# Performance work log

Measured on AMD Instinct MI355X. Metric: run time of the kernel, lower is better.

## Reference

```python
import jax, jax.numpy as jnp
import numpy as np
import math

D_HEAD = 64  # scaling uses sqrt(d_head), NOT sqrt of full projection dim (faithful to source)

def setup_inputs() -> dict:
    key = jax.random.key(0)
    ks = jax.random.split(key, 9)
    B, S, D = 4, 2048, 1024
    s = 0.02
    return {
        "x": jax.random.normal(ks[0], (B, S, D), dtype=jnp.float32),
        "Wq": jax.random.normal(ks[1], (D, D), dtype=jnp.float32) * s,
        "bq": jax.random.normal(ks[2], (D,), dtype=jnp.float32) * s,
        "Wk": jax.random.normal(ks[3], (D, D), dtype=jnp.float32) * s,
        "bk": jax.random.normal(ks[4], (D,), dtype=jnp.float32) * s,
        "Wv": jax.random.normal(ks[5], (D, D), dtype=jnp.float32) * s,
        "bv": jax.random.normal(ks[6], (D,), dtype=jnp.float32) * s,
        "Wo": jax.random.normal(ks[7], (D, D), dtype=jnp.float32) * s,
        "bo": jax.random.normal(ks[8], (D,), dtype=jnp.float32) * s,
    }

def reference(x, Wq, bq, Wk, bk, Wv, bv, Wo, bo):
    # Q/K/V projections: [B,S,D] @ [D,D] + b
    Q = jnp.einsum('bsd,de->bse', x, Wq) + bq
    K = jnp.einsum('bsd,de->bse', x, Wk) + bk
    V = jnp.einsum('bsd,de->bse', x, Wv) + bv
    # NOTE: source does bmm over the FULL projected dim (no head split),
    # scaled by sqrt(d_head) only.
    scores = jnp.einsum('bqd,bkd->bqk', Q, K) / math.sqrt(D_HEAD)  # [B,S,S]
    S_len = scores.shape[-1]
    causal = jnp.tril(jnp.ones((S_len, S_len), dtype=bool))
    scores = jnp.where(causal, scores, -jnp.inf)
    weights = jax.nn.softmax(scores, axis=-1)
    attn_out = jnp.einsum('bqk,bkd->bqd', weights, V)
    return jnp.einsum('bsd,de->bse', attn_out, Wo) + bo
```

## Files before the change

kernel.cpp:

```cpp
#include <hip/hip_runtime.h>
#include <stdint.h>

typedef _Float16 f16;
typedef __attribute__((ext_vector_type(8))) _Float16 f16x8;
typedef __attribute__((ext_vector_type(4))) _Float16 f16x4;
typedef __attribute__((ext_vector_type(4))) float f32x4;

#define BK 32

typedef __attribute__((address_space(3))) uint32_t lds_u32;
typedef const __attribute__((address_space(1))) uint32_t glb_u32;

__device__ __forceinline__ void gload_lds16(const void* g, void* l) {
    __builtin_amdgcn_global_load_lds((glb_u32*)g, (lds_u32*)l, 16, 0, 0);
}

template<int OUT_MODE, int CAUSAL, int TM, int TN>
__device__ __forceinline__
void gemm_body(const f16* __restrict__ A, const f16* __restrict__ B,
               const float* __restrict__ bias, const float* __restrict__ bias2,
               void* __restrict__ Cv, void* __restrict__ C2,
               int M, int N, int K,
               long long sAb, long long sBb, long long sCb, float scale,
               int bx, int by, int bzi)
{
    constexpr int IM = TM / 32;
    constexpr int JN = TN / 32;

    int mtile, n0;
    if (CAUSAL == 1) {
        int rem = bx, mi = 0;
        while (rem > mi) { rem -= mi + 1; ++mi; }
        mtile = mi;
        n0 = rem * TN;
    } else {
        mtile = by;
        n0 = bx * TN;
    }

    const int tid  = threadIdx.x;
    const int wave = tid >> 6;
    const int lane = tid & 63;
    const long long bz = bzi;
    A += bz * sAb;
    B += bz * sBb;

    __shared__ f16 As[TM * BK];
    __shared__ f16 Bs[TN * BK];

    const int srow  = lane >> 2;
    const int scolS = (((lane & 3) ^ ((srow >> 1) & 3))) * 8;
    const int fr    = lane & 15;
    const int fkS   = (((lane >> 4) ^ ((fr >> 1) & 3))) * 8;

    const int wm = (wave >> 1) * (TM / 2);
    const int wn = (wave & 1) * (TN / 2);

    const int npass = (CAUSAL == 2) ? 2 : 1;
    for (int pass = 0; pass < npass; ++pass) {
        const int mt = (CAUSAL == 2 && pass == 1) ? (M / TM - 1 - mtile) : mtile;
        const int m0 = mt * TM;
        const int Kend = (CAUSAL == 2) ? (m0 + TM) : K;

        f32x4 acc[IM][JN] = {};

        for (int k0 = 0; k0 < Kend; k0 += BK) {
            #pragma unroll
            for (int gg = 0; gg < TM / 64; ++gg) {
                const int g = wave * (TM / 64) + gg;
                gload_lds16(A + (long long)(m0 + g * 16 + srow) * K + (k0 + scolS),
                            &As[g * 512]);
            }
            #pragma unroll
            for (int gg = 0; gg < TN / 64; ++gg) {
                const int g = wave * (TN / 64) + gg;
                gload_lds16(B + (long long)(n0 + g * 16 + srow) * K + (k0 + scolS),
                            &Bs[g * 512]);
            }
            __syncthreads();

            f16x8 af[IM], bf[JN];
            #pragma unroll
            for (int i = 0; i < IM; ++i)
                af[i] = *(const f16x8*)&As[(wm + i * 16 + fr) * BK + fkS];
            #pragma unroll
            for (int j = 0; j < JN; ++j)
                bf[j] = *(const f16x8*)&Bs[(wn + j * 16 + fr) * BK + fkS];

            #pragma unroll
            for (int i = 0; i < IM; ++i)
                #pragma unroll
                for (int j = 0; j < JN; ++j)
                    acc[i][j] = __builtin_amdgcn_mfma_f32_16x16x32_f16(af[i], bf[j], acc[i][j], 0, 0, 0);
            __syncthreads();
        }

        const int cn = lane & 15;
        const int cm = (lane >> 4) * 4;
        #pragma unroll
        for (int j = 0; j < JN; ++j) {
            const int gn = n0 + wn + j * 16 + cn;
            #pragma unroll
            for (int i = 0; i < IM; ++i) {
                const int gm = m0 + wm + i * 16 + cm;
                if (OUT_MODE == 0) {
                    const float bv = bias ? bias[gn] : 0.f;
                    float* C = (float*)Cv + bz * sCb;
                    #pragma unroll
                    for (int r = 0; r < 4; ++r)
                        C[(long long)(gm + r) * N + gn] = acc[i][j][r] * scale + bv;
                } else {
                    const float bv = bias ? bias[(long long)bz * N + gn] : 0.f;
                    f16* C = (f16*)Cv + bz * sCb;
                    #pragma unroll
                    for (int r = 0; r < 4; ++r)
                        C[(long long)(gm + r) * N + gn] = (f16)(acc[i][j][r] * scale + bv);
                }
            }
        }
        if (CAUSAL == 2) __syncthreads();
    }
}


template<int ROWS>
__device__ __forceinline__
void stage2(const f16* __restrict__ G, int ldg, f16* lds,
            int grow0, int k0, int tid)
{
    const int l = tid & 63, w = tid >> 6;
    #pragma unroll
    for (int q = 0; q < ROWS / 32; ++q) {
        const int r = q * 32 + w * 8 + (l >> 3);
        const int csw = (((l & 7) ^ (r & 7)) << 3);
        gload_lds16(G + (long long)(grow0 + r) * ldg + (k0 + csw),
                    lds + q * 2048 + w * 512);
    }
}

template<int OUT_MODE, int CAUSAL, int TM, int TN>
__device__ __forceinline__
void gemm2_body(const f16* __restrict__ A, const f16* __restrict__ B,
                const float* __restrict__ bias, void* __restrict__ Cv,
                int M, int N, int K,
                long long sAb, long long sBb, long long sCb, float scale,
                int bx, int by, int bzi)
{
    constexpr int IM = TM / 32;
    constexpr int JN = TN / 32;

    int mtile, n0;
    if (CAUSAL == 1) {
        int rem = bx, mi = 0;
        while (rem > mi) { rem -= mi + 1; ++mi; }
        mtile = mi;
        n0 = rem * TN;
    } else {
        mtile = by;
        n0 = bx * TN;
    }

    const int tid  = threadIdx.x;
    const int wave = tid >> 6;
    const int lane = tid & 63;
    const long long bz = bzi;
    A += bz * sAb;
    B += bz * sBb;

    __shared__ f16 As[2][TM * 64];
    __shared__ f16 Bs[2][TN * 64];

    const int fr  = lane & 15;
    const int hk  = lane >> 4;
    const int lsw = lane & 7;
    const int wm  = (wave >> 1) * (TM / 2);
    const int wn  = (wave & 1) * (TN / 2);

    const int npass = (CAUSAL == 2) ? 2 : 1;
    for (int pass = 0; pass < npass; ++pass) {
        const int mt = (CAUSAL == 2 && pass == 1) ? (M / TM - 1 - mtile) : mtile;
        const int m0 = mt * TM;
        const int Kend = (CAUSAL == 2) ? (m0 + TM) : K;

        f32x4 acc[IM][JN] = {};

        stage2<TM>(A, K, &As[0][0], m0, 0, tid);
        stage2<TN>(B, K, &Bs[0][0], n0, 0, tid);
        asm volatile("s_waitcnt vmcnt(0)" ::: "memory");
        __builtin_amdgcn_s_barrier();

        int cur = 0;
        for (int k0 = 0; k0 < Kend; k0 += 64) {
            if (k0 + 64 < Kend) {
                stage2<TM>(A, K, &As[cur ^ 1][0], m0, k0 + 64, tid);
                stage2<TN>(B, K, &Bs[cur ^ 1][0], n0, k0 + 64, tid);
            }

            f16x8 af[IM][2], bf[JN][2];
            #pragma unroll
            for (int i = 0; i < IM; ++i)
                #pragma unroll
                for (int kk = 0; kk < 2; ++kk)
                    af[i][kk] = *(const f16x8*)((const char*)&As[cur][0] +
                        ((wm + i * 16 + fr) << 7) +
                        ((((kk << 2) | hk) ^ lsw) << 4));
            #pragma unroll
            for (int j = 0; j < JN; ++j)
                #pragma unroll
                for (int kk = 0; kk < 2; ++kk)
                    bf[j][kk] = *(const f16x8*)((const char*)&Bs[cur][0] +
                        ((wn + j * 16 + fr) << 7) +
                        ((((kk << 2) | hk) ^ lsw) << 4));

            asm volatile("s_waitcnt lgkmcnt(0)" ::: "memory");
            __builtin_amdgcn_s_setprio(1);
            #pragma unroll
            for (int i = 0; i < IM; ++i)
                #pragma unroll
                for (int j = 0; j < JN; ++j)
                    #pragma unroll
                    for (int kk = 0; kk < 2; ++kk)
                        acc[i][j] = __builtin_amdgcn_mfma_f32_16x16x32_f16(
                            af[i][kk], bf[j][kk], acc[i][j], 0, 0, 0);
            __builtin_amdgcn_s_setprio(0);

            asm volatile("s_waitcnt vmcnt(0)" ::: "memory");
            __builtin_amdgcn_s_barrier();
            cur ^= 1;
        }

        const int cn = lane & 15;
        const int cm = (lane >> 4) * 4;
        #pragma unroll
        for (int j = 0; j < JN; ++j) {
            const int gn = n0 + wn + j * 16 + cn;
            #pragma unroll
            for (int i = 0; i < IM; ++i) {
                const int gm = m0 + wm + i * 16 + cm;
                if (OUT_MODE == 0) {
                    const float bv = bias ? bias[gn] : 0.f;
                    float* C = (float*)Cv + bz * sCb;
                    #pragma unroll
                    for (int r = 0; r < 4; ++r)
                        C[(long long)(gm + r) * N + gn] = acc[i][j][r] * scale + bv;
                } else {
                    const float bv = bias ? bias[(long long)bz * N + gn] : 0.f;
                    f16* C = (f16*)Cv + bz * sCb;
                    #pragma unroll
                    for (int r = 0; r < 4; ++r)
                        C[(long long)(gm + r) * N + gn] = (f16)(acc[i][j][r] * scale + bv);
                }
            }
        }
    }
}

template<int OUT_MODE, int CAUSAL, int TM, int TN>
__global__ __launch_bounds__(256, 2)
void gemm2_bt(const f16* __restrict__ A, const f16* __restrict__ B,
              const float* __restrict__ bias, void* __restrict__ Cv,
              int M, int N, int K,
              long long sAb, long long sBb, long long sCb, float scale)
{
    gemm2_body<OUT_MODE, CAUSAL, TM, TN>(A, B, bias, Cv, M, N, K,
                                         sAb, sBb, sCb, scale,
                                         blockIdx.x, blockIdx.y, blockIdx.z);
}

__device__ __forceinline__
void stage_half(const f16* __restrict__ G, int ldg, f16* lds_half,
                int grow0, int k0, int tid)
{
    const int lr  = tid >> 3;
    const int csw = ((tid & 7) * 8) ^ ((lr & 7) << 3);
    gload_lds16(G + (long long)(grow0 + lr) * ldg + (k0 + csw),
                lds_half + ((tid >> 6) << 9));
    gload_lds16(G + (long long)(grow0 + 64 + lr) * ldg + (k0 + csw),
                lds_half + 4096 + ((tid >> 6) << 9));
}

__global__ __launch_bounds__(512, 2)
void gemm_proj_8ph(const f16* __restrict__ A, const f16* __restrict__ B,
                   const float* __restrict__ bvo,
                   f16* __restrict__ Qh, f16* __restrict__ Vt,
                   int M, int N, int K)
{
    (void)M;
    __shared__ f16 As[2][16384];
    __shared__ f16 Bs[2][16384];

    const int nwg  = gridDim.x;
    const int orig = blockIdx.x;
    const int swz  = (orig & 7) * (nwg >> 3) + (orig >> 3);
    const int ntn  = N >> 8;
    const int mt = swz / ntn, nt = swz - mt * ntn;
    const int m0 = mt << 8, n0 = nt << 8;

    const int tid  = threadIdx.x;
    const int lane = tid & 63;
    const int wave = tid >> 6;
    const int wm = (wave >> 2) << 7;
    const int wn = (wave & 3) << 6;
    const int fr  = lane & 15;
    const int hk  = lane >> 4;
    const int lsw = lane & 7;
    const int nkt = K >> 6;

    f32x4 acc[8][4] = {};
    f16x8 bf[4][2];

    stage_half(A, K, &As[0][0],    m0,       0, tid);
    stage_half(A, K, &As[0][8192], m0 + 128, 0, tid);
    stage_half(B, K, &Bs[0][0],    n0,       0, tid);
    stage_half(B, K, &Bs[0][8192], n0 + 128, 0, tid);
    if (nkt > 1) {
        stage_half(B, K, &Bs[1][0],    n0,       64, tid);
        stage_half(B, K, &Bs[1][8192], n0 + 128, 64, tid);
        asm volatile("s_waitcnt vmcnt(4)" ::: "memory");
    } else {
        asm volatile("s_waitcnt vmcnt(0)" ::: "memory");
    }
    __builtin_amdgcn_s_barrier();

    for (int t = 0; t < nkt; ++t) {
        const f16* Ab = As[t & 1];
        const f16* Bb = Bs[t & 1];
        #pragma unroll
        for (int p = 0; p < 4; ++p) {
            if (p == 0) {
                #pragma unroll
                for (int j = 0; j < 4; ++j)
                    #pragma unroll
                    for (int kk = 0; kk < 2; ++kk)
                        bf[j][kk] = *(const f16x8*)((const char*)Bb +
                            ((wn + j * 16 + fr) << 7) +
                            ((((kk << 2) | hk) ^ lsw) << 4));
            }
            f16x8 af[2][2];
            #pragma unroll
            for (int ii = 0; ii < 2; ++ii)
                #pragma unroll
                for (int kk = 0; kk < 2; ++kk)
                    af[ii][kk] = *(const f16x8*)((const char*)Ab +
                        ((wm + (2 * p + ii) * 16 + fr) << 7) +
                        ((((kk << 2) | hk) ^ lsw) << 4));

            if (p == 0 && t + 1 < nkt)
                stage_half(A, K, &As[(t + 1) & 1][0],    m0,       (t + 1) << 6, tid);
            if (p == 1 && t + 1 < nkt)
                stage_half(A, K, &As[(t + 1) & 1][8192], m0 + 128, (t + 1) << 6, tid);
            if (p == 2 && t + 2 < nkt)
                stage_half(B, K, &Bs[t & 1][0],          n0,       (t + 2) << 6, tid);
            if (p == 3 && t + 2 < nkt)
                stage_half(B, K, &Bs[t & 1][8192],       n0 + 128, (t + 2) << 6, tid);

            if (p == 0) asm volatile("s_waitcnt lgkmcnt(8)" ::: "memory");
            __builtin_amdgcn_s_barrier();
            asm volatile("s_waitcnt lgkmcnt(0)" ::: "memory");
            __builtin_amdgcn_s_setprio(1);
            #pragma unroll
            for (int ii = 0; ii < 2; ++ii)
                #pragma unroll
                for (int j = 0; j < 4; ++j)
                    #pragma unroll
                    for (int kk = 0; kk < 2; ++kk)
                        acc[2 * p + ii][j] = __builtin_amdgcn_mfma_f32_16x16x32_f16(
                            af[ii][kk], bf[j][kk], acc[2 * p + ii][j], 0, 0, 0);
            __builtin_amdgcn_s_setprio(0);
            if (p == 3) {
                if (t + 2 < nkt) asm volatile("s_waitcnt vmcnt(4)" ::: "memory");
                else             asm volatile("s_waitcnt vmcnt(0)" ::: "memory");
            }
            __builtin_amdgcn_s_barrier();
        }
    }

    const int cn  = lane & 15;
    const int cm4 = (lane >> 4) * 4;
    #pragma unroll
    for (int j = 0; j < 4; ++j) {
        const int gn  = n0 + wn + j * 16 + cn;
        const int sel = gn >> 10;
        const int nn  = gn & 1023;
        #pragma unroll
        for (int i = 0; i < 8; ++i) {
            const int gm = m0 + wm + i * 16 + cm4;
            if (sel == 0) {
                #pragma unroll
                for (int r = 0; r < 4; ++r)
                    Qh[(long long)(gm + r) * 1024 + nn] = (f16)acc[i][j][r];
            } else {
                const float bb = bvo[nn];
                const int b = gm >> 11, s = gm & 2047;
                f16x4 pk;
                #pragma unroll
                for (int r = 0; r < 4; ++r)
                    pk[r] = (f16)(acc[i][j][r] + bb);
                *(f16x4*)&Vt[(long long)b * 2097152 + (long long)nn * 2048 + s] = pk;
            }
        }
    }
}

__global__ __launch_bounds__(256)
void prep(const float* __restrict__ x,  const float* __restrict__ Wq,
          const float* __restrict__ bq, const float* __restrict__ Wk,
          const float* __restrict__ Wv, const float* __restrict__ bv,
          const float* __restrict__ Wo,
          f16* __restrict__ xb,  f16* __restrict__ Wqf, f16* __restrict__ Wkf,
          f16* __restrict__ Wvf, f16* __restrict__ Wot,
          float* __restrict__ bvo, float* __restrict__ wvec)
{
    __shared__ f16 tile[32][33];
    __shared__ float red[4][64];
    const int t = threadIdx.x;
    int id = blockIdx.x;

    if (id < 8192) {
        const int i = (id * 256 + t) * 4;
        const float4 v = *(const float4*)&x[i];
        f16x4 o; o[0]=(f16)v.x; o[1]=(f16)v.y; o[2]=(f16)v.z; o[3]=(f16)v.w;
        *(f16x4*)&xb[i] = o;
        return;
    }
    id -= 8192;
    if (id < 3072) {
        const float* src = (id < 1024) ? Wq : (id < 2048) ? Wk : Wv;
        f16* dst = (id < 1024) ? Wqf : (id < 2048) ? Wkf : Wvf;
        const int i = ((id & 1023) * 256 + t) * 4;
        const float4 v = *(const float4*)&src[i];
        f16x4 o; o[0]=(f16)v.x; o[1]=(f16)v.y; o[2]=(f16)v.z; o[3]=(f16)v.w;
        *(f16x4*)&dst[i] = o;
        return;
    }
    id -= 3072;
    if (id < 1024) {
        const int bx = (id & 31) * 32, by = (id >> 5) * 32;
        const int tx = t & 31, ty = t >> 5;
        #pragma unroll
        for (int i = 0; i < 32; i += 8)
            tile[ty + i][tx] = (f16)Wo[(long long)(by + ty + i) * 1024 + (bx + tx)];
        __syncthreads();
        #pragma unroll
        for (int i = 0; i < 32; i += 8)
            Wot[(long long)(bx + ty + i) * 1024 + (by + tx)] = tile[tx][ty + i];
        return;
    }
    id -= 1024;
    if (id < 16) {
        const int e0 = id * 64;
        const int wave = t >> 6, lane = t & 63;
        float acc = 0.f;
        for (int i = 0; i < 256; ++i) {
            const int k = wave * 256 + i;
            acc += bv[k] * Wo[(long long)k * 1024 + e0 + lane];
        }
        red[wave][lane] = acc;
        __syncthreads();
        if (wave == 0)
            bvo[e0 + lane] = red[0][lane] + red[1][lane] + red[2][lane] + red[3][lane];
        return;
    }
    id -= 16;
    {
        const int row = id * 4 + (t >> 6);
        const int lane = t & 63;
        const float* src = Wk + (long long)row * 1024;
        float a = 0.f;
        #pragma unroll
        for (int tt = 0; tt < 16; ++tt) a += src[lane + 64 * tt] * bq[lane + 64 * tt];
        #pragma unroll
        for (int o = 32; o > 0; o >>= 1) a += __shfl_down(a, o);
        if (lane == 0) wvec[row] = a * 0.125f;
    }
}

__global__ __launch_bounds__(256, 2)
void dual_weights_cvec(const f16* __restrict__ Wkf, const f16* __restrict__ Wqf,
                       const f16* __restrict__ Wot, const f16* __restrict__ Wvf,
                       f16* __restrict__ Wcat2,
                       const f16* __restrict__ xb, const float* __restrict__ wvec,
                       float* __restrict__ cbias)
{
    if (blockIdx.z == 2) {
        const int flat = blockIdx.y * 16 + blockIdx.x;
        const int wave = threadIdx.x >> 6, lane = threadIdx.x & 63;
        #pragma unroll
        for (int rr = 0; rr < 8; ++rr) {
            const int row = (flat * 4 + wave) * 8 + rr;
            const f16* src = xb + (long long)row * 1024;
            float a = 0.f;
            #pragma unroll
            for (int tt = 0; tt < 16; ++tt)
                a += (float)src[lane + 64 * tt] * wvec[lane + 64 * tt];
            #pragma unroll
            for (int o = 32; o > 0; o >>= 1) a += __shfl_down(a, o);
            if (lane == 0) cbias[row] = a;
        }
        return;
    }
    const f16* Ax = (blockIdx.z == 0) ? Wkf : Wot;
    const f16* Bx = (blockIdx.z == 0) ? Wqf : Wvf;
    f16* Cx = Wcat2 + (long long)blockIdx.z * 1024 * 1024;
    gemm_body<1, 0, 64, 64>(Ax, Bx, nullptr, nullptr, Cx, nullptr,
                            1024, 1024, 1024, 0, 0, 0, 1.f,
                            blockIdx.x, blockIdx.y, 0);
}

__global__ __launch_bounds__(256)
void softmax_causal(const f16* __restrict__ Sc, f16* __restrict__ P, int S)
{
    const long long row = blockIdx.x;
    const int q = (int)(row % S);
    const f16* src = Sc + row * S;
    f16* dst = P + row * S;
    const int t = threadIdx.x;
    __shared__ float redm[4], reds[4];

    f16x8 vv = {};
    if (t * 8 <= q) vv = *(const f16x8*)&src[t * 8];
    float v[8];
    float mx = -3.0e38f;
    #pragma unroll
    for (int i = 0; i < 8; ++i) {
        const int k = t * 8 + i;
        v[i] = (float)vv[i];
        if (k <= q) mx = fmaxf(mx, v[i]);
    }
    #pragma unroll
    for (int o = 32; o > 0; o >>= 1) mx = fmaxf(mx, __shfl_down(mx, o));
    if ((t & 63) == 0) redm[t >> 6] = mx;
    __syncthreads();
    mx = fmaxf(fmaxf(redm[0], redm[1]), fmaxf(redm[2], redm[3]));

    float sum = 0.f;
    #pragma unroll
    for (int i = 0; i < 8; ++i) {
        const int k = t * 8 + i;
        v[i] = (k <= q) ? __expf(v[i] - mx) : 0.f;
        sum += v[i];
    }
    #pragma unroll
    for (int o = 32; o > 0; o >>= 1) sum += __shfl_down(sum, o);
    if ((t & 63) == 0) reds[t >> 6] = sum;
    __syncthreads();
    sum = reds[0] + reds[1] + reds[2] + reds[3];
    const float inv = 1.f / sum;
    f16x8 ov;
    #pragma unroll
    for (int i = 0; i < 8; ++i) ov[i] = (f16)(v[i] * inv);
    *(f16x8*)&dst[t * 8] = ov;
}

extern "C" void kernel_launch(void* const* d_in, const int* in_sizes, int n_in,
                              void* d_out, int out_size, void* d_ws, size_t ws_size,
                              hipStream_t stream)
{
    const float* x  = (const float*)d_in[0];
    const float* Wq = (const float*)d_in[1];
    const float* bq = (const float*)d_in[2];
    const float* Wk = (const float*)d_in[3];
    const float* Wv = (const float*)d_in[5];
    const float* bv = (const float*)d_in[6];
    const float* Wo = (const float*)d_in[7];
    const float* bo = (const float*)d_in[8];
    float* out = (float*)d_out;

    const int B = 4, S = 2048, D = 1024;
    const long long SD  = (long long)S * D;
    const long long SS  = (long long)S * S;
    const long long BSD = (long long)B * SD;
    const int MS = B * S;

    char* p = (char*)d_ws;
    f16*   xb    = (f16*)p;  p += BSD * 2;
    f16*   Wqf   = (f16*)p;  p += (long long)D * D * 2;
    f16*   Wkf   = (f16*)p;  p += (long long)D * D * 2;
    f16*   Wvf   = (f16*)p;  p += (long long)D * D * 2;
    f16*   Wot   = (f16*)p;  p += (long long)D * D * 2;
    f16*   Wcat2 = (f16*)p;  p += 2LL * D * D * 2;
    float* bvo   = (float*)p; p += D * 4;
    float* wvec  = (float*)p; p += D * 4;
    float* cbias = (float*)p; p += (long long)MS * 4;
    f16*   Qh    = (f16*)p;  p += BSD * 2;
    f16*   Vt    = (f16*)p;  p += BSD * 2;
    f16*   Sc    = (f16*)p;  p += (long long)B * SS * 2;
    f16*   Pb    = (f16*)p;  p += (long long)B * SS * 2;

    dim3 blk(256);

    prep<<<dim3(12560), blk, 0, stream>>>(x, Wq, bq, Wk, Wv, bv, Wo,
                                          xb, Wqf, Wkf, Wvf, Wot, bvo, wvec);

    dual_weights_cvec<<<dim3(16, 16, 3), blk, 0, stream>>>(Wkf, Wqf, Wot, Wvf,
                                                           Wcat2, xb, wvec, cbias);

    dim3 gproj((MS / 256) * (2 * D / 256));
    gemm_proj_8ph<<<gproj, dim3(512), 0, stream>>>(xb, Wcat2, bvo, Qh, Vt,
                                                   MS, 2 * D, D);

    dim3 gsc(136, 1, B);
    gemm2_bt<1, 1, 128, 128><<<gsc, blk, 0, stream>>>(Qh, xb, cbias, Sc,
                                                      S, S, D, SD, SD, SS, 0.125f);

    softmax_causal<<<dim3((unsigned)(B * S)), blk, 0, stream>>>(Sc, Pb, S);

    dim3 gpv(D / 64, S / 128 / 2, B);
    gemm2_bt<0, 2, 128, 64><<<gpv, blk, 0, stream>>>(Pb, Vt, bo, out,
                                                     S, D, S, SS, SD, SD, 1.f);
}
```

Measured before the change: 269.7 us.

## Use 256x256 tile kernel for causal score GEMM and larger weight-fusion tiles

Generalizes the 256x256 projection GEMM kernel into a templated kernel with a causal triangular-tile mode, and uses it for the QK^T score GEMM instead of the 128x128 tiled kernel. The weight-product GEMM in dual_weights_cvec moves from the single-buffered 64x64 tile path to the double-buffered 128x128 path, with a matching grid and cvec row split. Softmax now skips writing probabilities beyond the 128-aligned causal boundary, and the bvo reduction uses four accumulators. Larger score tiles give more reuse, but with 144 blocks there may be fewer workgroups than the GPU can keep busy, and diagonal tiles do more masked work.

Result: faster. 250.7 us (-7.1%).

```diff
diff --git a/kernel.cpp b/kernel.cpp
--- a/kernel.cpp
+++ b/kernel.cpp
@@ -6,8 +6,6 @@
 typedef __attribute__((ext_vector_type(4))) _Float16 f16x4;
 typedef __attribute__((ext_vector_type(4))) float f32x4;
 
-#define BK 32
-
 typedef __attribute__((address_space(3))) uint32_t lds_u32;
 typedef const __attribute__((address_space(1))) uint32_t glb_u32;
 
@@ -15,14 +13,29 @@
     __builtin_amdgcn_global_load_lds((glb_u32*)g, (lds_u32*)l, 16, 0, 0);
 }
 
+
+template<int ROWS>
+__device__ __forceinline__
+void stage2(const f16* __restrict__ G, int ldg, f16* lds,
+            int grow0, int k0, int tid)
+{
+    const int l = tid & 63, w = tid >> 6;
+    #pragma unroll
+    for (int q = 0; q < ROWS / 32; ++q) {
+        const int r = q * 32 + w * 8 + (l >> 3);
+        const int csw = (((l & 7) ^ (r & 7)) << 3);
+        gload_lds16(G + (long long)(grow0 + r) * ldg + (k0 + csw),
+                    lds + q * 2048 + w * 512);
+    }
+}
+
 template<int OUT_MODE, int CAUSAL, int TM, int TN>
 __device__ __forceinline__
-void gemm_body(const f16* __restrict__ A, const f16* __restrict__ B,
-               const float* __restrict__ bias, const float* __restrict__ bias2,
-               void* __restrict__ Cv, void* __restrict__ C2,
-               int M, int N, int K,
-               long long sAb, long long sBb, long long sCb, float scale,
-               int bx, int by, int bzi)
+void gemm2_body(const f16* __restrict__ A, const f16* __restrict__ B,
+                const float* __restrict__ bias, void* __restrict__ Cv,
+                int M, int N, int K,
+                long long sAb, long long sBb, long long sCb, float scale,
+                int bx, int by, int bzi)
 {
     constexpr int IM = TM / 32;
     constexpr int JN = TN / 32;
@@ -45,128 +58,6 @@
     A += bz * sAb;
     B += bz * sBb;
 
-    __shared__ f16 As[TM * BK];
-    __shared__ f16 Bs[TN * BK];
-
-    const int srow  = lane >> 2;
-    const int scolS = (((lane & 3) ^ ((srow >> 1) & 3))) * 8;
-    const int fr    = lane & 15;
-    const int fkS   = (((lane >> 4) ^ ((fr >> 1) & 3))) * 8;
-
-    const int wm = (wave >> 1) * (TM / 2);
-    const int wn = (wave & 1) * (TN / 2);
-
-    const int npass = (CAUSAL == 2) ? 2 : 1;
-    for (int pass = 0; pass < npass; ++pass) {
-        const int mt = (CAUSAL == 2 && pass == 1) ? (M / TM - 1 - mtile) : mtile;
-        const int m0 = mt * TM;
-        const int Kend = (CAUSAL == 2) ? (m0 + TM) : K;
-
-        f32x4 acc[IM][JN] = {};
-
-        for (int k0 = 0; k0 < Kend; k0 += BK) {
-            #pragma unroll
-            for (int gg = 0; gg < TM / 64; ++gg) {
-                const int g = wave * (TM / 64) + gg;
-                gload_lds16(A + (long long)(m0 + g * 16 + srow) * K + (k0 + scolS),
-                            &As[g * 512]);
-            }
-            #pragma unroll
-            for (int gg = 0; gg < TN / 64; ++gg) {
-                const int g = wave * (TN / 64) + gg;
-                gload_lds16(B + (long long)(n0 + g * 16 + srow) * K + (k0 + scolS),
-                            &Bs[g * 512]);
-            }
-            __syncthreads();
-
-            f16x8 af[IM], bf[JN];
-            #pragma unroll
-            for (int i = 0; i < IM; ++i)
-                af[i] = *(const f16x8*)&As[(wm + i * 16 + fr) * BK + fkS];
-            #pragma unroll
-            for (int j = 0; j < JN; ++j)
-                bf[j] = *(const f16x8*)&Bs[(wn + j * 16 + fr) * BK + fkS];
-
-            #pragma unroll
-            for (int i = 0; i < IM; ++i)
-                #pragma unroll
-                for (int j = 0; j < JN; ++j)
-                    acc[i][j] = __builtin_amdgcn_mfma_f32_16x16x32_f16(af[i], bf[j], acc[i][j], 0, 0, 0);
-            __syncthreads();
-        }
-
-        const int cn = lane & 15;
-        const int cm = (lane >> 4) * 4;
-        #pragma unroll
-        for (int j = 0; j < JN; ++j) {
-            const int gn = n0 + wn + j * 16 + cn;
-            #pragma unroll
-            for (int i = 0; i < IM; ++i) {
-                const int gm = m0 + wm + i * 16 + cm;
-                if (OUT_MODE == 0) {
-                    const float bv = bias ? bias[gn] : 0.f;
-                    float* C = (float*)Cv + bz * sCb;
-                    #pragma unroll
-                    for (int r = 0; r < 4; ++r)
-                        C[(long long)(gm + r) * N + gn] = acc[i][j][r] * scale + bv;
-                } else {
-                    const float bv = bias ? bias[(long long)bz * N + gn] : 0.f;
-                    f16* C = (f16*)Cv + bz * sCb;
-                    #pragma unroll
-                    for (int r = 0; r < 4; ++r)
-                        C[(long long)(gm + r) * N + gn] = (f16)(acc[i][j][r] * scale + bv);
-                }
-            }
-        }
-        if (CAUSAL == 2) __syncthreads();
-    }
-}
-
-
-template<int ROWS>
-__device__ __forceinline__
-void stage2(const f16* __restrict__ G, int ldg, f16* lds,
-            int grow0, int k0, int tid)
-{
-    const int l = tid & 63, w = tid >> 6;
-    #pragma unroll
-    for (int q = 0; q < ROWS / 32; ++q) {
-        const int r = q * 32 + w * 8 + (l >> 3);
-        const int csw = (((l & 7) ^ (r & 7)) << 3);
-        gload_lds16(G + (long long)(grow0 + r) * ldg + (k0 + csw),
-                    lds + q * 2048 + w * 512);
-    }
-}
-
-template<int OUT_MODE, int CAUSAL, int TM, int TN>
-__device__ __forceinline__
-void gemm2_body(const f16* __restrict__ A, const f16* __restrict__ B,
-                const float* __restrict__ bias, void* __restrict__ Cv,
-                int M, int N, int K,
-                long long sAb, long long sBb, long long sCb, float scale,
-                int bx, int by, int bzi)
-{
-    constexpr int IM = TM / 32;
-    constexpr int JN = TN / 32;
-
-    int mtile, n0;
-    if (CAUSAL == 1) {
-        int rem = bx, mi = 0;
-        while (rem > mi) { rem -= mi + 1; ++mi; }
-        mtile = mi;
-        n0 = rem * TN;
-    } else {
-        mtile = by;
-        n0 = bx * TN;
-    }
-
-    const int tid  = threadIdx.x;
-    const int wave = tid >> 6;
-    const int lane = tid & 63;
-    const long long bz = bzi;
-    A += bz * sAb;
-    B += bz * sBb;
-
     __shared__ f16 As[2][TM * 64];
     __shared__ f16 Bs[2][TN * 64];
 
@@ -267,6 +158,7 @@
                                          blockIdx.x, blockIdx.y, blockIdx.z);
 }
 
+
 __device__ __forceinline__
 void stage_half(const f16* __restrict__ G, int ldg, f16* lds_half,
                 int grow0, int k0, int tid)
@@ -279,22 +171,39 @@
                 lds_half + 4096 + ((tid >> 6) << 9));
 }
 
+template<int MODE>
 __global__ __launch_bounds__(512, 2)
-void gemm_proj_8ph(const f16* __restrict__ A, const f16* __restrict__ B,
-                   const float* __restrict__ bvo,
-                   f16* __restrict__ Qh, f16* __restrict__ Vt,
-                   int M, int N, int K)
-{
-    (void)M;
+void gemm256_4ph(const f16* __restrict__ A, const f16* __restrict__ B,
+                 const float* __restrict__ bias, const float* __restrict__ bias2,
+                 f16* __restrict__ C0, f16* __restrict__ C1,
+                 int M, int N, int K,
+                 long long sAb, long long sBb, long long sCb, float scale)
+{
     __shared__ f16 As[2][16384];
     __shared__ f16 Bs[2][16384];
 
     const int nwg  = gridDim.x;
     const int orig = blockIdx.x;
     const int swz  = (orig & 7) * (nwg >> 3) + (orig >> 3);
-    const int ntn  = N >> 8;
-    const int mt = swz / ntn, nt = swz - mt * ntn;
-    const int m0 = mt << 8, n0 = nt << 8;
+
+    int m0, n0;
+    long long bz = 0;
+    if (MODE == 1) {
+        const int nr  = M >> 8;
+        const int per = nr * (nr + 1) / 2;
+        bz = swz / per;
+        int rem = swz - (int)bz * per, mi = 0;
+        while (rem > mi) { rem -= mi + 1; ++mi; }
+        m0 = mi << 8;
+        n0 = rem << 8;
+    } else {
+        const int ntn = N >> 8;
+        const int mt = swz / ntn, nt = swz - mt * ntn;
+        m0 = mt << 8;
+        n0 = nt << 8;
+    }
+    A += bz * sAb;
+    B += bz * sBb;
 
     const int tid  = threadIdx.x;
     const int lane = tid & 63;
@@ -379,24 +288,36 @@
     const int cm4 = (lane >> 4) * 4;
     #pragma unroll
     for (int j = 0; j < 4; ++j) {
-        const int gn  = n0 + wn + j * 16 + cn;
-        const int sel = gn >> 10;
-        const int nn  = gn & 1023;
-        #pragma unroll
-        for (int i = 0; i < 8; ++i) {
-            const int gm = m0 + wm + i * 16 + cm4;
-            if (sel == 0) {
+        const int gn = n0 + wn + j * 16 + cn;
+        if (MODE == 3) {
+            const int sel = gn >> 10;
+            const int nn  = gn & 1023;
+            #pragma unroll
+            for (int i = 0; i < 8; ++i) {
+                const int gm = m0 + wm + i * 16 + cm4;
+                if (sel == 0) {
+                    #pragma unroll
+                    for (int r = 0; r < 4; ++r)
+                        C0[(long long)(gm + r) * 1024 + nn] = (f16)acc[i][j][r];
+                } else {
+                    const float bb = bias2[nn];
+                    const int b = gm >> 11, s = gm & 2047;
+                    f16x4 pk;
+                    #pragma unroll
+                    for (int r = 0; r < 4; ++r)
+                        pk[r] = (f16)(acc[i][j][r] + bb);
+                    *(f16x4*)&C1[(long long)b * 2097152 + (long long)nn * 2048 + s] = pk;
+                }
+            }
+        } else {
+            const float cbv = bias ? bias[bz * N + gn] : 0.f;
+            f16* Cc = C0 + bz * sCb;
+            #pragma unroll
+            for (int i = 0; i < 8; ++i) {
+                const int gm = m0 + wm + i * 16 + cm4;
                 #pragma unroll
                 for (int r = 0; r < 4; ++r)
-                    Qh[(long long)(gm + r) * 1024 + nn] = (f16)acc[i][j][r];
-            } else {
-                const float bb = bvo[nn];
-                const int b = gm >> 11, s = gm & 2047;
-                f16x4 pk;
-                #pragma unroll
-                for (int r = 0; r < 4; ++r)
-                    pk[r] = (f16)(acc[i][j][r] + bb);
-                *(f16x4*)&Vt[(long long)b * 2097152 + (long long)nn * 2048 + s] = pk;
+                    Cc[(long long)(gm + r) * N + gn] = (f16)(acc[i][j][r] * scale + cbv);
             }
         }
     }
@@ -450,12 +371,15 @@
     if (id < 16) {
         const int e0 = id * 64;
         const int wave = t >> 6, lane = t & 63;
-        float acc = 0.f;
-        for (int i = 0; i < 256; ++i) {
+        float a0 = 0.f, a1 = 0.f, a2 = 0.f, a3 = 0.f;
+        for (int i = 0; i < 256; i += 4) {
             const int k = wave * 256 + i;
-            acc += bv[k] * Wo[(long long)k * 1024 + e0 + lane];
+            a0 += bv[k]     * Wo[(long long)k * 1024 + e0 + lane];
+            a1 += bv[k + 1] * Wo[(long long)(k + 1) * 1024 + e0 + lane];
+            a2 += bv[k + 2] * Wo[(long long)(k + 2) * 1024 + e0 + lane];
+            a3 += bv[k + 3] * Wo[(long long)(k + 3) * 1024 + e0 + lane];
         }
-        red[wave][lane] = acc;
+        red[wave][lane] = (a0 + a1) + (a2 + a3);
         __syncthreads();
         if (wave == 0)
             bvo[e0 + lane] = red[0][lane] + red[1][lane] + red[2][lane] + red[3][lane];
@@ -483,11 +407,11 @@
                        float* __restrict__ cbias)
 {
     if (blockIdx.z == 2) {
-        const int flat = blockIdx.y * 16 + blockIdx.x;
+        const int flat = blockIdx.y * 8 + blockIdx.x;
         const int wave = threadIdx.x >> 6, lane = threadIdx.x & 63;
-        #pragma unroll
-        for (int rr = 0; rr < 8; ++rr) {
-            const int row = (flat * 4 + wave) * 8 + rr;
+        #pragma unroll 4
+        for (int rr = 0; rr < 32; ++rr) {
+            const int row = (flat * 4 + wave) * 32 + rr;
             const f16* src = xb + (long long)row * 1024;
             float a = 0.f;
             #pragma unroll
@@ -502,9 +426,9 @@
     const f16* Ax = (blockIdx.z == 0) ? Wkf : Wot;
     const f16* Bx = (blockIdx.z == 0) ? Wqf : Wvf;
     f16* Cx = Wcat2 + (long long)blockIdx.z * 1024 * 1024;
-    gemm_body<1, 0, 64, 64>(Ax, Bx, nullptr, nullptr, Cx, nullptr,
-                            1024, 1024, 1024, 0, 0, 0, 1.f,
-                            blockIdx.x, blockIdx.y, 0);
+    gemm2_body<1, 0, 128, 128>(Ax, Bx, nullptr, Cx,
+                               1024, 1024, 1024, 0, 0, 0, 1.f,
+                               blockIdx.x, blockIdx.y, 0);
 }
 
 __global__ __launch_bounds__(256)
@@ -546,10 +470,13 @@
     __syncthreads();
     sum = reds[0] + reds[1] + reds[2] + reds[3];
     const float inv = 1.f / sum;
-    f16x8 ov;
-    #pragma unroll
-    for (int i = 0; i < 8; ++i) ov[i] = (f16)(v[i] * inv);
-    *(f16x8*)&dst[t * 8] = ov;
+    const int kend = ((q >> 7) + 1) << 7;
+    if (t * 8 < kend) {
+        f16x8 ov;
+        #pragma unroll
+        for (int i = 0; i < 8; ++i) ov[i] = (f16)(v[i] * inv);
+        *(f16x8*)&dst[t * 8] = ov;
+    }
 }
 
 extern "C" void kernel_launch(void* const* d_in, const int* in_sizes, int n_in,
@@ -592,16 +519,18 @@
     prep<<<dim3(12560), blk, 0, stream>>>(x, Wq, bq, Wk, Wv, bv, Wo,
                                           xb, Wqf, Wkf, Wvf, Wot, bvo, wvec);
 
-    dual_weights_cvec<<<dim3(16, 16, 3), blk, 0, stream>>>(Wkf, Wqf, Wot, Wvf,
-                                                           Wcat2, xb, wvec, cbias);
+    dual_weights_cvec<<<dim3(8, 8, 3), blk, 0, stream>>>(Wkf, Wqf, Wot, Wvf,
+                                                         Wcat2, xb, wvec, cbias);
 
     dim3 gproj((MS / 256) * (2 * D / 256));
-    gemm_proj_8ph<<<gproj, dim3(512), 0, stream>>>(xb, Wcat2, bvo, Qh, Vt,
-                                                   MS, 2 * D, D);
-
-    dim3 gsc(136, 1, B);
-    gemm2_bt<1, 1, 128, 128><<<gsc, blk, 0, stream>>>(Qh, xb, cbias, Sc,
-                                                      S, S, D, SD, SD, SS, 0.125f);
+    gemm256_4ph<3><<<gproj, dim3(512), 0, stream>>>(xb, Wcat2, nullptr, bvo,
+                                                    Qh, Vt,
+                                                    MS, 2 * D, D, 0, 0, 0, 1.f);
+
+    dim3 gsc(144);
+    gemm256_4ph<1><<<gsc, dim3(512), 0, stream>>>(Qh, xb, cbias, nullptr,
+                                                  Sc, nullptr,
+                                                  S, S, D, SD, SD, SS, 0.125f);
 
     softmax_causal<<<dim3((unsigned)(B * S)), blk, 0, stream>>>(Sc, Pb, S);
 
```
